# Kernel tuning notes

Hardware: AMD Instinct MI355X
Metric: run time of the kernel (lower is better)

## Reference

```python
import jax, jax.numpy as jnp
import numpy as np

B, S, D, H, WIN = 2, 2048, 1024, 16, 512
DK = D // H
NEG_INF = float('-inf')


def setup_inputs() -> dict:
    key = jax.random.key(0)
    ks = jax.random.split(key, 9)
    sc = 1.0 / np.sqrt(D)
    def w(k):
        return jax.random.normal(k, (D, D), jnp.float32) * sc
    def b(k):
        return jax.random.normal(k, (D,), jnp.float32) * 0.01
    return {
        'x': jax.random.normal(ks[0], (B, S, D), jnp.float32),
        'Wq_w': w(ks[1]), 'Wq_b': b(jax.random.fold_in(ks[1], 1)),
        'Wk_w': w(ks[2]), 'Wk_b': b(jax.random.fold_in(ks[2], 1)),
        'Wv_w': w(ks[3]), 'Wv_b': b(jax.random.fold_in(ks[3], 1)),
        'Wo_w': w(ks[4]), 'Wo_b': b(jax.random.fold_in(ks[4], 1)),
    }


def _sliding_window_softmax(scores):
    """Faithful port of _apply_sliding_window_attention.

    scores: [B, H, S, S]. seq_len is a multiple of WIN (padding_len == 0,
    which is the only case where the original torch code runs without a
    shape error). Reshape rows/cols into WIN-sized blocks, apply the full
    causal mask (viewed block-wise), softmax over the within-window key
    axis, reshape back. Rows whose entire window block is masked produce
    NaN in torch; here they are defined as 0 (safe softmax) so the
    reference is numerically usable.
    """
    b, h, s, _ = scores.shape
    nb = s // WIN
    causal = jnp.tril(jnp.ones((s, s), dtype=bool)).reshape(1, 1, nb, WIN, nb, WIN)
    sc = scores.reshape(b, h, nb, WIN, nb, WIN)
    sc = jnp.where(causal, sc, NEG_INF)
    m = jnp.max(sc, axis=-1, keepdims=True)
    e = jnp.exp(sc - jnp.where(jnp.isfinite(m), m, 0.0))
    e = jnp.where(causal, e, 0.0)
    denom = jnp.sum(e, axis=-1, keepdims=True)
    probs = e / jnp.where(denom == 0.0, 1.0, denom)
    return probs.reshape(b, h, s, s)


def reference(x, Wq_w, Wq_b, Wk_w, Wk_b, Wv_w, Wv_b, Wo_w, Wo_b):
    b, s, d = x.shape
    # torch nn.Linear: y = x @ W.T + b
    q = (x @ Wq_w.T + Wq_b).reshape(b, s, H, DK).transpose(0, 2, 1, 3)  # [B,H,S,DK]
    k = (x @ Wk_w.T + Wk_b).reshape(b, s, H, DK).transpose(0, 2, 1, 3)
    v = (x @ Wv_w.T + Wv_b).reshape(b, s, H, DK).transpose(0, 2, 1, 3)

    attn_scores = jnp.einsum('bhqd,bhkd->bhqk', q, k) / np.sqrt(DK)  # [B,H,S,S]
    if WIN < s:  # sliding-window branch (window softmax, as in the source)
        attn_scores = _sliding_window_softmax(attn_scores)
    # second, full-row softmax (the source applies softmax again)
    attn_probs = jax.nn.softmax(attn_scores, axis=-1)
    attn_out = jnp.einsum('bhqk,bhkd->bhqd', attn_probs, v)
    attn_out = attn_out.transpose(0, 2, 1, 3).reshape(b, s, d)
    return attn_out @ Wo_w.T + Wo_b
```

## Files before the change

### kernel.cpp

```cpp
#include <hip/hip_runtime.h>
#include <hip/hip_bf16.h>

typedef short v8s __attribute__((ext_vector_type(8)));
typedef float v4f __attribute__((ext_vector_type(4)));
typedef unsigned int v4u __attribute__((ext_vector_type(4)));
typedef unsigned int v2u __attribute__((ext_vector_type(2)));

#define DEV static __device__ __forceinline__

DEV float bf2f(unsigned short u){ unsigned int x=((unsigned int)u)<<16; float f; __builtin_memcpy(&f,&x,4); return f; }
DEV short f2bf(float f){ __hip_bfloat16 h=__float2bfloat16(f); short s; __builtin_memcpy(&s,&h,2); return s; }
DEV unsigned int f2bfu(float f){ unsigned int u; __builtin_memcpy(&u,&f,4); return (u + 0x7fffu + ((u>>16)&1u)) >> 16; }
DEV unsigned int pk2(float a, float b){ return f2bfu(a) | (f2bfu(b)<<16); }
DEV v4f mfma16(v8s a, v8s b, v4f c){ return __builtin_amdgcn_mfma_f32_16x16x32_bf16(a,b,c,0,0,0); }

__global__ __launch_bounds__(256) void convert_kernel(
    const float* __restrict__ x,  const float* __restrict__ Wq,
    const float* __restrict__ Wk, const float* __restrict__ Wv,
    short* __restrict__ xb, short* __restrict__ wqb,
    short* __restrict__ wkb, short* __restrict__ wvb)
{
  unsigned g = blockIdx.x*256u + threadIdx.x;
  const float* src; short* dst; unsigned off;
  if (g < 1048576u){ src=x;  dst=xb;  off=g; }
  else if (g < 1310720u){ src=Wq; dst=wqb; off=g-1048576u; }
  else if (g < 1572864u){ src=Wk; dst=wkb; off=g-1310720u; }
  else { src=Wv; dst=wvb; off=g-1572864u; }
  v4f f = *(const v4f*)(src + (size_t)off*4);
  v2u r; r[0]=pk2(f[0],f[1]); r[1]=pk2(f[2],f[3]);
  *(v2u*)(dst + (size_t)off*4) = r;
}

template<int BF32>
DEV void gemm_core(const short* __restrict__ A, const void* __restrict__ Bmat,
                   int brow0, int bn0, int tid, short* As, short* Bs, v4f acc[4][4])
{
  const int l = tid & 63, w = tid >> 6;
  const int wr = (w>>1)*64, wc = (w&1)*64;
  const short* B16 = (const short*)Bmat;
  const float* B32 = (const float*)Bmat;
  for (int kt=0; kt<32; ++kt){
    v4u ra0, ra1, rb0, rb1;
    {
      int idx=tid;      int row=idx>>2, p=idx&3;
      ra0 = *(const v4u*)(A + (size_t)(brow0+row)*1024 + kt*32 + (p^((row>>1)&3))*8);
      idx=tid+256;      row=idx>>2; p=idx&3;
      ra1 = *(const v4u*)(A + (size_t)(brow0+row)*1024 + kt*32 + (p^((row>>1)&3))*8);
      if (BF32){
        idx=tid;        row=idx>>2; p=idx&3;
        {
          const float* s0 = B32 + (size_t)(bn0+row)*1024 + kt*32 + (p^((row>>1)&3))*8;
          v4f f0=*(const v4f*)s0, f1=*(const v4f*)(s0+4);
          rb0[0]=pk2(f0[0],f0[1]); rb0[1]=pk2(f0[2],f0[3]);
          rb0[2]=pk2(f1[0],f1[1]); rb0[3]=pk2(f1[2],f1[3]);
        }
        idx=tid+256;    row=idx>>2; p=idx&3;
        {
          const float* s1 = B32 + (size_t)(bn0+row)*1024 + kt*32 + (p^((row>>1)&3))*8;
          v4f f0=*(const v4f*)s1, f1=*(const v4f*)(s1+4);
          rb1[0]=pk2(f0[0],f0[1]); rb1[1]=pk2(f0[2],f0[3]);
          rb1[2]=pk2(f1[0],f1[1]); rb1[3]=pk2(f1[2],f1[3]);
        }
      } else {
        int idx2=tid;   int row=idx2>>2, p=idx2&3;
        rb0 = *(const v4u*)(B16 + (size_t)(bn0+row)*1024 + kt*32 + (p^((row>>1)&3))*8);
        idx2=tid+256;   row=idx2>>2; p=idx2&3;
        rb1 = *(const v4u*)(B16 + (size_t)(bn0+row)*1024 + kt*32 + (p^((row>>1)&3))*8);
      }
    }
    __syncthreads();
    *(v4u*)&As[(size_t)tid*8]       = ra0;
    *(v4u*)&As[(size_t)(tid+256)*8] = ra1;
    *(v4u*)&Bs[(size_t)tid*8]       = rb0;
    *(v4u*)&Bs[(size_t)(tid+256)*8] = rb1;
    __syncthreads();
    v8s af[4], bfr[4];
    #pragma unroll
    for (int m=0;m<4;++m){ int r=wr+m*16+(l&15); af[m]=*(const v8s*)&As[(r*4+((l>>4)^((r>>1)&3)))*8]; }
    #pragma unroll
    for (int n=0;n<4;++n){ int r=wc+n*16+(l&15); bfr[n]=*(const v8s*)&Bs[(r*4+((l>>4)^((r>>1)&3)))*8]; }
    #pragma unroll
    for (int m=0;m<4;++m)
      #pragma unroll
      for (int n=0;n<4;++n)
        acc[m][n]=mfma16(af[m],bfr[n],acc[m][n]);
  }
}

__global__ __launch_bounds__(256) void qkv_gemm(const short* __restrict__ xb,
    const short* __restrict__ wqb, const short* __restrict__ wkb, const short* __restrict__ wvb,
    const float* __restrict__ bq, const float* __restrict__ bk, const float* __restrict__ bv,
    short* __restrict__ qo, short* __restrict__ ko, short* __restrict__ vfo)
{
  __shared__ short As[4096], Bs[4096];
  const int tid=threadIdx.x, l=tid&63, w=tid>>6;
  const int bcol0=blockIdx.x*128, brow0=blockIdx.y*128;
  const int mat=bcol0>>10, n0=bcol0&1023;
  const short* Wm   = mat==0?wqb:(mat==1?wkb:wvb);
  const float* bias = mat==0?bq:(mat==1?bk:bv);
  v4f acc[4][4];
  v4f vz={0.f,0.f,0.f,0.f};
  #pragma unroll
  for(int m=0;m<4;++m)
    #pragma unroll
    for(int n=0;n<4;++n) acc[m][n]=vz;
  gemm_core<0>(xb, Wm, brow0, n0, tid, As, Bs, acc);
  const int wr=(w>>1)*64, wc=(w&1)*64;
  #pragma unroll
  for(int m=0;m<4;++m)
  #pragma unroll
  for(int n=0;n<4;++n)
  #pragma unroll
  for(int r=0;r<4;++r){
    int row=brow0+wr+m*16+(l>>4)*4+r;
    int col=n0+wc+n*16+(l&15);
    float v=acc[m][n][r]+bias[col];
    int b=row>>11, s=row&2047, h=col>>6, dk=col&63;
    int bh=b*16+h;
    short sv=f2bf(v);
    if(mat==0)      qo[((size_t)bh*2048+s)*64+dk]=sv;
    else if(mat==1) ko[((size_t)bh*2048+s)*64+dk]=sv;
    else{
      int kb=s>>9, c=(s>>5)&15, ki=s&31;
      int g2=(ki>>2)&3, j=(ki>>4)*4+(ki&3);
      int lane2=g2*16+(dk&15);
      vfo[((((size_t)bh*4+kb)*16+c)*4+(size_t)(dk>>4))*512 + lane2*8 + j]=sv;
    }
  }
}

__global__ __launch_bounds__(64) void vbsum_kernel(const short* __restrict__ vf, float* __restrict__ vbp)
{
  const int bh=blockIdx.x, kb=blockIdx.y, l=threadIdx.x;
  const short* base = vf + ((size_t)(bh*4+kb))*16*4*512;
  float acc[4]={0.f,0.f,0.f,0.f};
  #pragma unroll
  for(int c=0;c<16;++c)
    #pragma unroll
    for(int dt=0;dt<4;++dt){
      v8s vv=*(const v8s*)(base + ((size_t)(c*4+dt))*512 + l*8);
      float s=0.f;
      #pragma unroll
      for(int j=0;j<8;++j) s+=bf2f((unsigned short)vv[j]);
      acc[dt]+=s;
    }
  #pragma unroll
  for(int dt=0;dt<4;++dt){
    acc[dt]+=__shfl_xor(acc[dt],16);
    acc[dt]+=__shfl_xor(acc[dt],32);
  }
  if(l<16){
    #pragma unroll
    for(int dt=0;dt<4;++dt) vbp[(size_t)(bh*4+kb)*64 + dt*16 + l]=acc[dt];
  }
}

__global__ __launch_bounds__(256) void attn_kernel(
  const short* __restrict__ q, const short* __restrict__ k, const short* __restrict__ vf,
  const float* __restrict__ vbp, short* __restrict__ attn)
{
  __shared__ short kbuf[16384];
  __shared__ float d1buf[256];
  const int tid=threadIdx.x, l=tid&63, wv=tid>>6;
  const int bh=blockIdx.x, qt=31-blockIdx.y;
  const int qb=qt>>3;
  const int qrow0=qt*64+wv*16;
  const int g=l>>4, q16=l&15;
  const int b=bh>>4, h=bh&15;
  const int qglob=qrow0+q16;
  const int lrow=wv*16+q16;

  const short* qbase = q + (size_t)bh*2048*64;
  const short* kbase = k + (size_t)bh*2048*64;
  const short* qp = qbase + (size_t)(qrow0+q16)*64 + g*8;
  v8s qa0=*(const v8s*)qp, qa1=*(const v8s*)(qp+32);
  v4f vz={0.f,0.f,0.f,0.f};

  auto stage=[&](int kb2,int hb2){
    #pragma unroll
    for (int i=0;i<8;++i){
      int idx=i*256+tid, key=idx>>3, p=idx&7, pp=p^(key&7);
      const short* gp = kbase + (size_t)(kb2*512+hb2*256+key)*64 + pp*8;
      __builtin_amdgcn_global_load_lds((const __attribute__((address_space(1))) void*)gp,
          (__attribute__((address_space(3))) void*)((char*)kbuf + idx*16), 16, 0, 0);
    }
  };

#define QKE(CT, EV)                                                     \
  v4f EV;                                                               \
  { int krow=((CT)&15)*16+q16;                                          \
    int s0=g^(krow&7), s1=(g+4)^(krow&7);                               \
    v8s k0=*(const v8s*)&kbuf[(krow*8+s0)*8];                           \
    v8s k1=*(const v8s*)&kbuf[(krow*8+s1)*8];                           \
    v4f t=mfma16(k0,qa0,vz);                                            \
    v4f e4=mfma16(k1,qa1,t);                                            \
    _Pragma("unroll")                                                   \
    for (int r=0;r<4;++r){                                              \
      float s=e4[r]*0.125f;                                             \
      if (diag && kb*512+(CT)*16+g*4+r > qglob) s=-1e38f;               \
      EV[r]=__expf(s);                                                  \
    }                                                                   \
  }

  for (int kb=0; kb<=qb; ++kb){
    const bool diag=(kb==qb);
    const int tmaxw = diag ? ((qt&7)*4+wv) : 31;
    const int blkhi = diag ? ((qt&7)*4+3) : 31;
    float d1acc=0.f;
    stage(kb,0); __syncthreads();
    #pragma unroll
    for (int ct=0;ct<16;++ct) if (ct<=tmaxw){
      QKE(ct,ev)
      d1acc+=(ev[0]+ev[1])+(ev[2]+ev[3]);
    }
    __syncthreads();
    if (blkhi>=16){
      stage(kb,1); __syncthreads();
      #pragma unroll
      for (int ct=16;ct<32;++ct) if (ct<=tmaxw){
        QKE(ct,ev)
        d1acc+=(ev[0]+ev[1])+(ev[2]+ev[3]);
      }
      __syncthreads();
    }
    float d1=d1acc;
    d1+=__shfl_xor(d1,16); d1+=__shfl_xor(d1,32);
    if (l<16) d1buf[(wv*16+l)*4+kb]=1.0f/d1;
  }
  __syncthreads();

  v4f o[4];
  #pragma unroll
  for(int dt=0;dt<4;++dt) o[dt]=vz;
  float zacc=0.f;

#define CHUNK(C)                                                        \
  { QKE(2*(C),eA) QKE(2*(C)+1,eB)                                       \
    float w0=__expf(eA[0]*d1i)-1.0f, w1=__expf(eA[1]*d1i)-1.0f;         \
    float w2=__expf(eA[2]*d1i)-1.0f, w3=__expf(eA[3]*d1i)-1.0f;         \
    float w4=__expf(eB[0]*d1i)-1.0f, w5=__expf(eB[1]*d1i)-1.0f;         \
    float w6=__expf(eB[2]*d1i)-1.0f, w7=__expf(eB[3]*d1i)-1.0f;         \
    zacc+=((w0+w1)+(w2+w3))+((w4+w5)+(w6+w7));                          \
    union { v4u u; v8s s; } pa;                                         \
    pa.u[0]=pk2(w0,w1); pa.u[1]=pk2(w2,w3);                             \
    pa.u[2]=pk2(w4,w5); pa.u[3]=pk2(w6,w7);                             \
    const short* vfp = vf + ((((size_t)bh*4+kb)*16+(C))*4)*512 + l*8;   \
    _Pragma("unroll")                                                   \
    for (int dt=0;dt<4;++dt){                                           \
      v8s vfr=*(const v8s*)(vfp + (size_t)dt*512);                      \
      o[dt]=mfma16(pa.s,vfr,o[dt]);                                     \
    }                                                                   \
  }

  for (int kb=0; kb<=qb; ++kb){
    const bool diag=(kb==qb);
    const int tmaxw = diag ? ((qt&7)*4+wv) : 31;
    const int blkhi = diag ? ((qt&7)*4+3) : 31;
    const float d1i=d1buf[lrow*4+kb];
    stage(kb,0); __syncthreads();
    #pragma unroll
    for (int c=0;c<8;++c) if (2*c<=tmaxw) CHUNK(c)
    __syncthreads();
    if (blkhi>=16){
      stage(kb,1); __syncthreads();
      #pragma unroll
      for (int c=8;c<16;++c) if (2*c<=tmaxw) CHUNK(c)
      __syncthreads();
    }
  }
#undef CHUNK
#undef QKE

  float z=zacc;
  z+=__shfl_xor(z,16); z+=__shfl_xor(z,32);
  float base[4];
  #pragma unroll
  for (int dt=0;dt<4;++dt){
    float s=0.f;
    #pragma unroll
    for (int kk=0;kk<4;++kk) s+=vbp[(size_t)(bh*4+kk)*64 + dt*16 + q16];
    base[dt]=s;
  }
  #pragma unroll
  for (int r=0;r<4;++r){
    float zr=__shfl(z, g*4+r);
    float inv=1.0f/(2048.0f+zr);
    int rowi=qrow0+g*4+r;
    size_t obase=((size_t)b*2048+rowi)*1024 + h*64;
    #pragma unroll
    for (int dt=0;dt<4;++dt)
      attn[obase + dt*16 + q16] = f2bf((o[dt][r]+base[dt])*inv);
  }
}

__global__ __launch_bounds__(256) void oproj_gemm(const short* __restrict__ at,
    const float* __restrict__ Wo, const float* __restrict__ bo, float* __restrict__ out)
{
  __shared__ short As[4096], Bs[4096];
  const int tid=threadIdx.x, l=tid&63, w=tid>>6;
  const int bcol0=blockIdx.x*128, brow0=blockIdx.y*128;
  v4f acc[4][4];
  v4f vz={0.f,0.f,0.f,0.f};
  #pragma unroll
  for(int m=0;m<4;++m)
    #pragma unroll
    for(int n=0;n<4;++n) acc[m][n]=vz;
  gemm_core<1>(at, Wo, brow0, bcol0, tid, As, Bs, acc);
  const int wr=(w>>1)*64, wc=(w&1)*64;
  #pragma unroll
  for(int m=0;m<4;++m)
  #pragma unroll
  for(int n=0;n<4;++n)
  #pragma unroll
  for(int r=0;r<4;++r){
    int row=brow0+wr+m*16+(l>>4)*4+r;
    int col=bcol0+wc+n*16+(l&15);
    out[(size_t)row*1024+col]=acc[m][n][r]+bo[col];
  }
}

extern "C" void kernel_launch(void* const* d_in, const int* in_sizes, int n_in,
                              void* d_out, int out_size, void* d_ws, size_t ws_size,
                              hipStream_t stream)
{
  const float* x  =(const float*)d_in[0];
  const float* Wq =(const float*)d_in[1];
  const float* bq =(const float*)d_in[2];
  const float* Wk =(const float*)d_in[3];
  const float* bk =(const float*)d_in[4];
  const float* Wv =(const float*)d_in[5];
  const float* bv =(const float*)d_in[6];
  const float* Wo =(const float*)d_in[7];
  const float* bo =(const float*)d_in[8];
  float* out=(float*)d_out;
  char* ws=(char*)d_ws;
  short* xb_ws =(short*)(ws);
  short* at_ws =(short*)(ws);
  short* q_ws  =(short*)(ws + ((size_t)8<<20));
  short* k_ws  =(short*)(ws + ((size_t)16<<20));
  short* vf_ws =(short*)(ws + ((size_t)24<<20));
  char*  outb  =(char*)d_out;
  short* wqb   =(short*)(outb);
  short* wkb   =(short*)(outb + ((size_t)2<<20));
  short* wvb   =(short*)(outb + ((size_t)4<<20));
  float* vbp_ws=(float*)(outb + ((size_t)7<<20));

  convert_kernel<<<dim3(7168),256,0,stream>>>(x,Wq,Wk,Wv,xb_ws,wqb,wkb,wvb);
  qkv_gemm<<<dim3(24,32),256,0,stream>>>(xb_ws,wqb,wkb,wvb,bq,bk,bv,q_ws,k_ws,vf_ws);
  vbsum_kernel<<<dim3(32,4),64,0,stream>>>(vf_ws,vbp_ws);
  attn_kernel<<<dim3(32,32),256,0,stream>>>(q_ws,k_ws,vf_ws,vbp_ws,at_ws);
  oproj_gemm<<<dim3(8,32),256,0,stream>>>(at_ws,Wo,bo,out);
}
```

Measured before the change: 176.0 us.

## Double-buffer QKV GEMM via LDS DMA, fold scale into Q, split diagonal attention

```diff
diff --git a/kernel.cpp b/kernel.cpp
--- a/kernel.cpp
+++ b/kernel.cpp
@@ -7,11 +7,14 @@
 typedef unsigned int v2u __attribute__((ext_vector_type(2)));
 
 #define DEV static __device__ __forceinline__
+#define AS1 __attribute__((address_space(1)))
+#define AS3 __attribute__((address_space(3)))
 
 DEV float bf2f(unsigned short u){ unsigned int x=((unsigned int)u)<<16; float f; __builtin_memcpy(&f,&x,4); return f; }
 DEV short f2bf(float f){ __hip_bfloat16 h=__float2bfloat16(f); short s; __builtin_memcpy(&s,&h,2); return s; }
 DEV unsigned int f2bfu(float f){ unsigned int u; __builtin_memcpy(&u,&f,4); return (u + 0x7fffu + ((u>>16)&1u)) >> 16; }
 DEV unsigned int pk2(float a, float b){ return f2bfu(a) | (f2bfu(b)<<16); }
+DEV unsigned int cvtpk(float lo, float hi){ unsigned r; asm("v_cvt_pk_bf16_f32 %0, %1, %2":"=v"(r):"v"(lo),"v"(hi)); return r; }
 DEV v4f mfma16(v8s a, v8s b, v4f c){ return __builtin_amdgcn_mfma_f32_16x16x32_bf16(a,b,c,0,0,0); }
 
 __global__ __launch_bounds__(256) void convert_kernel(
@@ -31,14 +34,50 @@
   *(v2u*)(dst + (size_t)off*4) = r;
 }
 
-template<int BF32>
-DEV void gemm_core(const short* __restrict__ A, const void* __restrict__ Bmat,
-                   int brow0, int bn0, int tid, short* As, short* Bs, v4f acc[4][4])
+DEV void gemm_core16(const short* __restrict__ A, const short* __restrict__ Bmat,
+                     int brow0, int bn0, int tid, short* As, short* Bs, v4f acc[4][4])
 {
   const int l = tid & 63, w = tid >> 6;
   const int wr = (w>>1)*64, wc = (w&1)*64;
-  const short* B16 = (const short*)Bmat;
-  const float* B32 = (const float*)Bmat;
+  const int row = tid>>2, p = tid&3;
+  const int sw = (p^((row>>1)&3))*8;
+  auto STAGE=[&](int kt,int buf){
+    const short* a0 = A    + (size_t)(brow0+row   )*1024 + kt*32 + sw;
+    const short* a1 = A    + (size_t)(brow0+row+64)*1024 + kt*32 + sw;
+    const short* b0 = Bmat + (size_t)(bn0 +row   )*1024 + kt*32 + sw;
+    const short* b1 = Bmat + (size_t)(bn0 +row+64)*1024 + kt*32 + sw;
+    __builtin_amdgcn_global_load_lds((const AS1 void*)a0,(AS3 void*)(As+buf*4096+(size_t)tid*8),16,0,0);
+    __builtin_amdgcn_global_load_lds((const AS1 void*)a1,(AS3 void*)(As+buf*4096+(size_t)(tid+256)*8),16,0,0);
+    __builtin_amdgcn_global_load_lds((const AS1 void*)b0,(AS3 void*)(Bs+buf*4096+(size_t)tid*8),16,0,0);
+    __builtin_amdgcn_global_load_lds((const AS1 void*)b1,(AS3 void*)(Bs+buf*4096+(size_t)(tid+256)*8),16,0,0);
+  };
+  STAGE(0,0);
+  asm volatile("s_waitcnt vmcnt(0)" ::: "memory");
+  __builtin_amdgcn_s_barrier();
+  int cur=0;
+  for (int kt=0; kt<32; ++kt){
+    if (kt<31) STAGE(kt+1,cur^1);
+    v8s af[4], bfr[4];
+    #pragma unroll
+    for (int m=0;m<4;++m){ int r=wr+m*16+(l&15); af[m]=*(const v8s*)&As[cur*4096+(r*4+((l>>4)^((r>>1)&3)))*8]; }
+    #pragma unroll
+    for (int n=0;n<4;++n){ int r=wc+n*16+(l&15); bfr[n]=*(const v8s*)&Bs[cur*4096+(r*4+((l>>4)^((r>>1)&3)))*8]; }
+    #pragma unroll
+    for (int m=0;m<4;++m)
+      #pragma unroll
+      for (int n=0;n<4;++n)
+        acc[m][n]=mfma16(af[m],bfr[n],acc[m][n]);
+    asm volatile("s_waitcnt vmcnt(0)" ::: "memory");
+    __builtin_amdgcn_s_barrier();
+    cur^=1;
+  }
+}
+
+DEV void gemm_core_f32(const short* __restrict__ A, const float* __restrict__ B32,
+                   int brow0, int bn0, int tid, short* As, short* Bs, v4f acc[4][4])
+{
+  const int l = tid & 63, w = tid >> 6;
+  const int wr = (w>>1)*64, wc = (w&1)*64;
   for (int kt=0; kt<32; ++kt){
     v4u ra0, ra1, rb0, rb1;
     {
@@ -46,26 +85,19 @@
       ra0 = *(const v4u*)(A + (size_t)(brow0+row)*1024 + kt*32 + (p^((row>>1)&3))*8);
       idx=tid+256;      row=idx>>2; p=idx&3;
       ra1 = *(const v4u*)(A + (size_t)(brow0+row)*1024 + kt*32 + (p^((row>>1)&3))*8);
-      if (BF32){
-        idx=tid;        row=idx>>2; p=idx&3;
-        {
-          const float* s0 = B32 + (size_t)(bn0+row)*1024 + kt*32 + (p^((row>>1)&3))*8;
-          v4f f0=*(const v4f*)s0, f1=*(const v4f*)(s0+4);
-          rb0[0]=pk2(f0[0],f0[1]); rb0[1]=pk2(f0[2],f0[3]);
-          rb0[2]=pk2(f1[0],f1[1]); rb0[3]=pk2(f1[2],f1[3]);
-        }
-        idx=tid+256;    row=idx>>2; p=idx&3;
-        {
-          const float* s1 = B32 + (size_t)(bn0+row)*1024 + kt*32 + (p^((row>>1)&3))*8;
-          v4f f0=*(const v4f*)s1, f1=*(const v4f*)(s1+4);
-          rb1[0]=pk2(f0[0],f0[1]); rb1[1]=pk2(f0[2],f0[3]);
-          rb1[2]=pk2(f1[0],f1[1]); rb1[3]=pk2(f1[2],f1[3]);
-        }
-      } else {
-        int idx2=tid;   int row=idx2>>2, p=idx2&3;
-        rb0 = *(const v4u*)(B16 + (size_t)(bn0+row)*1024 + kt*32 + (p^((row>>1)&3))*8);
-        idx2=tid+256;   row=idx2>>2; p=idx2&3;
-        rb1 = *(const v4u*)(B16 + (size_t)(bn0+row)*1024 + kt*32 + (p^((row>>1)&3))*8);
+      idx=tid;          row=idx>>2; p=idx&3;
+      {
+        const float* s0 = B32 + (size_t)(bn0+row)*1024 + kt*32 + (p^((row>>1)&3))*8;
+        v4f f0=*(const v4f*)s0, f1=*(const v4f*)(s0+4);
+        rb0[0]=pk2(f0[0],f0[1]); rb0[1]=pk2(f0[2],f0[3]);
+        rb0[2]=pk2(f1[0],f1[1]); rb0[3]=pk2(f1[2],f1[3]);
+      }
+      idx=tid+256;      row=idx>>2; p=idx&3;
+      {
+        const float* s1 = B32 + (size_t)(bn0+row)*1024 + kt*32 + (p^((row>>1)&3))*8;
+        v4f f0=*(const v4f*)s1, f1=*(const v4f*)(s1+4);
+        rb1[0]=pk2(f0[0],f0[1]); rb1[1]=pk2(f0[2],f0[3]);
+        rb1[2]=pk2(f1[0],f1[1]); rb1[3]=pk2(f1[2],f1[3]);
       }
     }
     __syncthreads();
@@ -92,7 +124,7 @@
     const float* __restrict__ bq, const float* __restrict__ bk, const float* __restrict__ bv,
     short* __restrict__ qo, short* __restrict__ ko, short* __restrict__ vfo)
 {
-  __shared__ short As[4096], Bs[4096];
+  __shared__ short As[8192], Bs[8192];
   const int tid=threadIdx.x, l=tid&63, w=tid>>6;
   const int bcol0=blockIdx.x*128, brow0=blockIdx.y*128;
   const int mat=bcol0>>10, n0=bcol0&1023;
@@ -104,8 +136,9 @@
   for(int m=0;m<4;++m)
     #pragma unroll
     for(int n=0;n<4;++n) acc[m][n]=vz;
-  gemm_core<0>(xb, Wm, brow0, n0, tid, As, Bs, acc);
+  gemm_core16(xb, Wm, brow0, n0, tid, As, Bs, acc);
   const int wr=(w>>1)*64, wc=(w&1)*64;
+  const float qscale = 0.18033688011112042f;
   #pragma unroll
   for(int m=0;m<4;++m)
   #pragma unroll
@@ -117,14 +150,13 @@
     float v=acc[m][n][r]+bias[col];
     int b=row>>11, s=row&2047, h=col>>6, dk=col&63;
     int bh=b*16+h;
-    short sv=f2bf(v);
-    if(mat==0)      qo[((size_t)bh*2048+s)*64+dk]=sv;
-    else if(mat==1) ko[((size_t)bh*2048+s)*64+dk]=sv;
+    if(mat==0)      qo[((size_t)bh*2048+s)*64+dk]=f2bf(v*qscale);
+    else if(mat==1) ko[((size_t)bh*2048+s)*64+dk]=f2bf(v);
     else{
       int kb=s>>9, c=(s>>5)&15, ki=s&31;
       int g2=(ki>>2)&3, j=(ki>>4)*4+(ki&3);
       int lane2=g2*16+(dk&15);
-      vfo[((((size_t)bh*4+kb)*16+c)*4+(size_t)(dk>>4))*512 + lane2*8 + j]=sv;
+      vfo[((((size_t)bh*4+kb)*16+c)*4+(size_t)(dk>>4))*512 + lane2*8 + j]=f2bf(v);
     }
   }
 }
@@ -181,12 +213,12 @@
     for (int i=0;i<8;++i){
       int idx=i*256+tid, key=idx>>3, p=idx&7, pp=p^(key&7);
       const short* gp = kbase + (size_t)(kb2*512+hb2*256+key)*64 + pp*8;
-      __builtin_amdgcn_global_load_lds((const __attribute__((address_space(1))) void*)gp,
-          (__attribute__((address_space(3))) void*)((char*)kbuf + idx*16), 16, 0, 0);
+      __builtin_amdgcn_global_load_lds((const AS1 void*)gp,
+          (AS3 void*)((char*)kbuf + idx*16), 16, 0, 0);
     }
   };
 
-#define QKE(CT, EV)                                                     \
+#define QKE(CT, EV, MASKED)                                             \
   v4f EV;                                                               \
   { int krow=((CT)&15)*16+q16;                                          \
     int s0=g^(krow&7), s1=(g+4)^(krow&7);                               \
@@ -196,36 +228,43 @@
     v4f e4=mfma16(k1,qa1,t);                                            \
     _Pragma("unroll")                                                   \
     for (int r=0;r<4;++r){                                              \
-      float s=e4[r]*0.125f;                                             \
-      if (diag && kb*512+(CT)*16+g*4+r > qglob) s=-1e38f;               \
-      EV[r]=__expf(s);                                                  \
+      float s=e4[r];                                                    \
+      if ((MASKED) && kb*512+(CT)*16+g*4+r > qglob) s=-1e38f;           \
+      EV[r]=exp2f(s);                                                   \
     }                                                                   \
   }
 
-  for (int kb=0; kb<=qb; ++kb){
-    const bool diag=(kb==qb);
-    const int tmaxw = diag ? ((qt&7)*4+wv) : 31;
-    const int blkhi = diag ? ((qt&7)*4+3) : 31;
+  for (int kb=0; kb<qb; ++kb){
     float d1acc=0.f;
     stage(kb,0); __syncthreads();
     #pragma unroll
-    for (int ct=0;ct<16;++ct) if (ct<=tmaxw){
-      QKE(ct,ev)
-      d1acc+=(ev[0]+ev[1])+(ev[2]+ev[3]);
-    }
+    for (int ct=0;ct<16;++ct){ QKE(ct,ev,false) d1acc+=(ev[0]+ev[1])+(ev[2]+ev[3]); }
+    __syncthreads();
+    stage(kb,1); __syncthreads();
+    #pragma unroll
+    for (int ct=16;ct<32;++ct){ QKE(ct,ev,false) d1acc+=(ev[0]+ev[1])+(ev[2]+ev[3]); }
+    __syncthreads();
+    float d1=d1acc;
+    d1+=__shfl_xor(d1,16); d1+=__shfl_xor(d1,32);
+    if (l<16) d1buf[(wv*16+l)*4+kb]=1.44269504f/d1;
+  }
+  {
+    const int kb=qb;
+    const int tmax=(qt&7)*4+wv, blkhi=(qt&7)*4+3;
+    float d1acc=0.f;
+    stage(kb,0); __syncthreads();
+    #pragma unroll
+    for (int ct=0;ct<16;++ct) if (ct<=tmax){ QKE(ct,ev,true) d1acc+=(ev[0]+ev[1])+(ev[2]+ev[3]); }
     __syncthreads();
     if (blkhi>=16){
       stage(kb,1); __syncthreads();
       #pragma unroll
-      for (int ct=16;ct<32;++ct) if (ct<=tmaxw){
-        QKE(ct,ev)
-        d1acc+=(ev[0]+ev[1])+(ev[2]+ev[3]);
-      }
+      for (int ct=16;ct<32;++ct) if (ct<=tmax){ QKE(ct,ev,true) d1acc+=(ev[0]+ev[1])+(ev[2]+ev[3]); }
       __syncthreads();
     }
     float d1=d1acc;
     d1+=__shfl_xor(d1,16); d1+=__shfl_xor(d1,32);
-    if (l<16) d1buf[(wv*16+l)*4+kb]=1.0f/d1;
+    if (l<16) d1buf[(wv*16+l)*4+kb]=1.44269504f/d1;
   }
   __syncthreads();
 
@@ -234,16 +273,16 @@
   for(int dt=0;dt<4;++dt) o[dt]=vz;
   float zacc=0.f;
 
-#define CHUNK(C)                                                        \
-  { QKE(2*(C),eA) QKE(2*(C)+1,eB)                                       \
-    float w0=__expf(eA[0]*d1i)-1.0f, w1=__expf(eA[1]*d1i)-1.0f;         \
-    float w2=__expf(eA[2]*d1i)-1.0f, w3=__expf(eA[3]*d1i)-1.0f;         \
-    float w4=__expf(eB[0]*d1i)-1.0f, w5=__expf(eB[1]*d1i)-1.0f;         \
-    float w6=__expf(eB[2]*d1i)-1.0f, w7=__expf(eB[3]*d1i)-1.0f;         \
+#define CHUNK(C, MASKED)                                                \
+  { QKE(2*(C),eA,MASKED) QKE(2*(C)+1,eB,MASKED)                         \
+    float w0=exp2f(eA[0]*d1i)-1.0f, w1=exp2f(eA[1]*d1i)-1.0f;           \
+    float w2=exp2f(eA[2]*d1i)-1.0f, w3=exp2f(eA[3]*d1i)-1.0f;           \
+    float w4=exp2f(eB[0]*d1i)-1.0f, w5=exp2f(eB[1]*d1i)-1.0f;           \
+    float w6=exp2f(eB[2]*d1i)-1.0f, w7=exp2f(eB[3]*d1i)-1.0f;           \
     zacc+=((w0+w1)+(w2+w3))+((w4+w5)+(w6+w7));                          \
     union { v4u u; v8s s; } pa;                                         \
-    pa.u[0]=pk2(w0,w1); pa.u[1]=pk2(w2,w3);                             \
-    pa.u[2]=pk2(w4,w5); pa.u[3]=pk2(w6,w7);                             \
+    pa.u[0]=cvtpk(w0,w1); pa.u[1]=cvtpk(w2,w3);                         \
+    pa.u[2]=cvtpk(w4,w5); pa.u[3]=cvtpk(w6,w7);                         \
     const short* vfp = vf + ((((size_t)bh*4+kb)*16+(C))*4)*512 + l*8;   \
     _Pragma("unroll")                                                   \
     for (int dt=0;dt<4;++dt){                                           \
@@ -252,19 +291,29 @@
     }                                                                   \
   }
 
-  for (int kb=0; kb<=qb; ++kb){
-    const bool diag=(kb==qb);
-    const int tmaxw = diag ? ((qt&7)*4+wv) : 31;
-    const int blkhi = diag ? ((qt&7)*4+3) : 31;
+  for (int kb=0; kb<qb; ++kb){
     const float d1i=d1buf[lrow*4+kb];
     stage(kb,0); __syncthreads();
     #pragma unroll
-    for (int c=0;c<8;++c) if (2*c<=tmaxw) CHUNK(c)
+    for (int c=0;c<8;++c) CHUNK(c,false)
+    __syncthreads();
+    stage(kb,1); __syncthreads();
+    #pragma unroll
+    for (int c=8;c<16;++c) CHUNK(c,false)
+    __syncthreads();
+  }
+  {
+    const int kb=qb;
+    const float d1i=d1buf[lrow*4+kb];
+    const int tmax=(qt&7)*4+wv, blkhi=(qt&7)*4+3;
+    stage(kb,0); __syncthreads();
+    #pragma unroll
+    for (int c=0;c<8;++c) if (2*c<=tmax) CHUNK(c,true)
     __syncthreads();
     if (blkhi>=16){
       stage(kb,1); __syncthreads();
       #pragma unroll
-      for (int c=8;c<16;++c) if (2*c<=tmaxw) CHUNK(c)
+      for (int c=8;c<16;++c) if (2*c<=tmax) CHUNK(c,true)
       __syncthreads();
     }
   }
@@ -305,7 +354,7 @@
   for(int m=0;m<4;++m)
     #pragma unroll
     for(int n=0;n<4;++n) acc[m][n]=vz;
-  gemm_core<1>(at, Wo, brow0, bcol0, tid, As, Bs, acc);
+  gemm_core_f32(at, Wo, brow0, bcol0, tid, As, Bs, acc);
   const int wr=(w>>1)*64, wc=(w&1)*64;
   #pragma unroll
   for(int m=0;m<4;++m)
```

Result: slower. 184.6 us (+4.9%).
